# Kernel optimization log

Measured on AMD Instinct MI355X. Metric: run time of the kernel, lower is better.

Reference implementation:

```python
import jax, jax.numpy as jnp
import numpy as np

B, T, D, H = 4, 2048, 1024, 16
HD = D // H  # head_dim = 64

def setup_inputs() -> dict:
    key = jax.random.key(0)
    k1, k2, k3 = jax.random.split(key, 3)
    scale_in = 1.0 / np.sqrt(D)
    return {
        "x": jax.random.normal(k1, (B, T, D), dtype=jnp.float32),
        "W_qkv": jax.random.normal(k2, (D, 3 * D), dtype=jnp.float32) * scale_in,
        "b_qkv": jnp.zeros((3 * D,), dtype=jnp.float32),
        "W_out": jax.random.normal(k3, (D, D), dtype=jnp.float32) * scale_in,
        "b_out": jnp.zeros((D,), dtype=jnp.float32),
    }

def reference(x, W_qkv, b_qkv, W_out, b_out):
    Bx, Tx, C = x.shape
    qkv = x @ W_qkv + b_qkv                      # [B,T,3D]
    q, k, v = jnp.split(qkv, 3, axis=-1)
    # [B,T,D] -> [B,H,T,hd]
    def to_heads(t):
        return t.reshape(Bx, Tx, H, HD).transpose(0, 2, 1, 3)
    q, k, v = to_heads(q), to_heads(k), to_heads(v)
    scores = jnp.einsum('bhqd,bhkd->bhqk', q, k) / np.sqrt(HD)  # [B,H,T,T]
    causal = jnp.tril(jnp.ones((Tx, Tx), dtype=bool))
    scores = jnp.where(causal, scores, -jnp.inf)
    attn = jax.nn.softmax(scores, axis=-1)       # dropout p=0 -> identity
    out = jnp.einsum('bhqk,bhkd->bhqd', attn, v)  # [B,H,T,hd]
    out = out.transpose(0, 2, 1, 3).reshape(Bx, Tx, C)
    return out @ W_out + b_out
```

## Files before the change

kernel.cpp:

```cpp
#include <hip/hip_runtime.h>
#include <hip/hip_bf16.h>

#define BB 4
#define TT 2048
#define DD 1024
#define HH 16
#define HDIM 64
#define BT (BB*TT)
#define D3 (3*DD)

typedef __attribute__((ext_vector_type(8))) short bf16x8;
typedef __attribute__((ext_vector_type(4))) float f32x4;

#if __has_builtin(__builtin_amdgcn_exp2f)
#define EXP2(x) __builtin_amdgcn_exp2f(x)
#else
#define EXP2(x) exp2f(x)
#endif

__device__ __forceinline__ ushort f2bf(float f) {
  union { float f; uint32_t u; } v; v.f = f;
  uint32_t u = v.u + 0x7FFFu + ((v.u >> 16) & 1u);
  return (ushort)(u >> 16);
}

__device__ __forceinline__ ushort f2bf_hw(float f) {
  __hip_bfloat16 h = __float2bfloat16(f);
  ushort u;
  __builtin_memcpy(&u, &h, 2);
  return u;
}

__device__ __forceinline__ float bf2f(ushort u) {
  union { uint32_t i; float f; } x; x.i = ((uint32_t)u) << 16; return x.f;
}

__device__ __forceinline__ void gload_lds16(const void* g, void* l) {
  __builtin_amdgcn_global_load_lds((const __attribute__((address_space(1))) void*)g,
                                   (__attribute__((address_space(3))) void*)l, 16, 0, 0);
}

__global__ __launch_bounds__(256)
void cvt_bf16(const float* __restrict__ in, ushort* __restrict__ out, int n4) {
  int i = blockIdx.x * blockDim.x + threadIdx.x;
  int stride = gridDim.x * blockDim.x;
  for (; i < n4; i += stride) {
    float4 v = ((const float4*)in)[i];
    ushort4 o;
    o.x = f2bf(v.x); o.y = f2bf(v.y); o.z = f2bf(v.z); o.w = f2bf(v.w);
    ((ushort4*)out)[i] = o;
  }
}

__global__ __launch_bounds__(256)
void transpose_cvt(const float* __restrict__ W, ushort* __restrict__ Wt, int K, int N) {
  __shared__ ushort Tt[64][68];
  const int n0 = blockIdx.x * 64;
  const int k0 = blockIdx.y * 64;
  const int tid = threadIdx.x;
  const int r = tid >> 4;
  const int c4 = (tid & 15) * 4;
  #pragma unroll
  for (int i = 0; i < 4; ++i) {
    int row = r + i * 16;
    float4 v = *(const float4*)&W[(size_t)(k0 + row) * N + n0 + c4];
    Tt[c4 + 0][row] = f2bf(v.x);
    Tt[c4 + 1][row] = f2bf(v.y);
    Tt[c4 + 2][row] = f2bf(v.z);
    Tt[c4 + 3][row] = f2bf(v.w);
  }
  __syncthreads();
  #pragma unroll
  for (int i = 0; i < 4; ++i) {
    int row = r + i * 16;
    ushort4 tv = *(const ushort4*)&Tt[row][c4];
    *(ushort4*)&Wt[(size_t)(n0 + row) * K + k0 + c4] = tv;
  }
}

template<bool F32OUT>
__global__ __launch_bounds__(256)
void gemm_bt(const ushort* __restrict__ A, const ushort* __restrict__ Bw,
             const float* __restrict__ bias, void* __restrict__ C, int N) {
  __shared__ __align__(16) short As[128 * 64];
  __shared__ __align__(16) short Bs[128 * 64];
  const int tid = threadIdx.x;
  const int w = tid >> 6, lane = tid & 63;
  const int li = lane & 15, g = lane >> 4;
  const int wm = w >> 1, wn = w & 1;
  const int bm = blockIdx.y * 128;
  const int bn = blockIdx.x * 128;
  const int lrow = lane >> 3;
  const int lchunk = lane & 7;

  f32x4 acc[4][4] = {};

  for (int k0 = 0; k0 < 1024; k0 += 64) {
    __syncthreads();
    #pragma unroll
    for (int j = 0; j < 4; ++j) {
      int row = j * 32 + w * 8 + lrow;
      gload_lds16(A  + (size_t)(bm + row) * 1024 + k0 + lchunk * 8, As + j * 2048 + w * 512);
      gload_lds16(Bw + (size_t)(bn + row) * 1024 + k0 + lchunk * 8, Bs + j * 2048 + w * 512);
    }
    __syncthreads();
    #pragma unroll
    for (int c = 0; c < 2; ++c) {
      bf16x8 af[4], bfr[4];
      #pragma unroll
      for (int mi = 0; mi < 4; ++mi)
        af[mi] = *(bf16x8*)&As[(wm * 64 + mi * 16 + li) * 64 + c * 32 + g * 8];
      #pragma unroll
      for (int ni = 0; ni < 4; ++ni)
        bfr[ni] = *(bf16x8*)&Bs[(wn * 64 + ni * 16 + li) * 64 + c * 32 + g * 8];
      #pragma unroll
      for (int mi = 0; mi < 4; ++mi)
        #pragma unroll
        for (int ni = 0; ni < 4; ++ni)
          acc[mi][ni] = __builtin_amdgcn_mfma_f32_16x16x32_bf16(af[mi], bfr[ni], acc[mi][ni], 0, 0, 0);
    }
  }
  #pragma unroll
  for (int ni = 0; ni < 4; ++ni) {
    int col = bn + wn * 64 + ni * 16 + li;
    float bv = bias[col];
    #pragma unroll
    for (int mi = 0; mi < 4; ++mi) {
      int row = bm + wm * 64 + mi * 16 + g * 4;
      #pragma unroll
      for (int r = 0; r < 4; ++r) {
        float v = acc[mi][ni][r] + bv;
        if (F32OUT) ((float*)C)[(size_t)(row + r) * N + col] = v;
        else        ((ushort*)C)[(size_t)(row + r) * N + col] = f2bf_hw(v);
      }
    }
  }
}

__global__ void zero_ctr(uint* c) { *c = 0u; }

#define NITEMS 1024

__global__ __launch_bounds__(256)
void attn_mfma(const ushort* __restrict__ qkv, ushort* __restrict__ out,
               uint* __restrict__ ctr) {
  __shared__ __align__(16) short Ks[64 * 64];
  __shared__ __align__(16) short Vt[64 * 64];
  __shared__ __align__(16) short Pl[4 * 16 * 64];
  __shared__ int s_item;

  const int tid = threadIdx.x;
  const int w = tid >> 6;
  const int lane = tid & 63;
  const int li = lane & 15, g = lane >> 4;
  const int sw = (li & 7) << 4;

  char* KsB = (char*)Ks;
  char* VtB = (char*)Vt;
  char* PlB = (char*)Pl + w * 2048;

  const int krow0 = tid >> 3;
  const int kc = tid & 7;
  const int d0 = (tid >> 5) * 8;
  const int kp = tid & 31;
  const int kswz = (kc * 16) ^ ((krow0 & 7) << 4);

  for (;;) {
    if (tid == 0) s_item = (int)atomicAdd(ctr, 1u);
    __syncthreads();
    const int item = s_item;
    if (item >= NITEMS) return;

    const int qt = 15 - (item >> 6);
    const int bh = item & 63;
    const int h = bh & 15, b = bh >> 4;
    const int qg0 = qt * 128 + w * 32;

    bf16x8 qfr[2][2];
    #pragma unroll
    for (int qf = 0; qf < 2; ++qf) {
      const ushort* qrow = qkv + (size_t)(b * TT + qg0 + qf * 16 + li) * D3 + h * HDIM;
      #pragma unroll
      for (int c = 0; c < 2; ++c) {
        uint4 raw = *(const uint4*)(qrow + c * 32 + g * 8);
        const ushort* rp = (const ushort*)&raw;
        bf16x8 v;
        #pragma unroll
        for (int j = 0; j < 8; ++j)
          v[j] = (short)f2bf_hw(bf2f(rp[j]) * 0.18033688f);
        qfr[qf][c] = v;
      }
    }

    f32x4 o[4][2] = {};
    float lsum[2] = {0.f, 0.f};

    const ushort* kbase = qkv + (size_t)b * TT * D3 + DD + h * HDIM;
    const ushort* vbase = kbase + DD;

    const int nt = 2 * qt + 2;
    const int itlast = 2 * qt + (w >> 1);

    uint4 kpre0, kpre1, vpre0, vpre1;
    {
      const ushort* kg = kbase + (size_t)krow0 * D3 + kc * 8;
      kpre0 = *(const uint4*)kg;
      kpre1 = *(const uint4*)(kg + (size_t)32 * D3);
      const ushort* vg = vbase + (size_t)(2 * kp) * D3 + d0;
      vpre0 = *(const uint4*)vg;
      vpre1 = *(const uint4*)(vg + D3);
    }

    for (int it = 0; it < nt; ++it) {
      const int k0 = it * 64;
      *(uint4*)(KsB + krow0 * 128 + kswz) = kpre0;
      *(uint4*)(KsB + (krow0 + 32) * 128 + kswz) = kpre1;
      {
        const ushort* pa = (const ushort*)&vpre0;
        const ushort* pb = (const ushort*)&vpre1;
        #pragma unroll
        for (int j = 0; j < 8; ++j) {
          uint32_t pk = (uint32_t)pa[j] | ((uint32_t)pb[j] << 16);
          *(uint32_t*)(VtB + (d0 + j) * 128 + ((4 * kp) ^ (j << 4))) = pk;
        }
      }
      __syncthreads();
      if (it + 1 < nt) {
        const ushort* kg = kbase + (size_t)(k0 + 64 + krow0) * D3 + kc * 8;
        kpre0 = *(const uint4*)kg;
        kpre1 = *(const uint4*)(kg + (size_t)32 * D3);
        const ushort* vg = vbase + (size_t)(k0 + 64 + 2 * kp) * D3 + d0;
        vpre0 = *(const uint4*)vg;
        vpre1 = *(const uint4*)(vg + D3);
      }
      if (it <= itlast) {
        const bool domask = (it == itlast);
        bf16x8 pf[2][2];
        f32x4 s[2][4];
        __builtin_amdgcn_s_setprio(1);
        #pragma unroll
        for (int kt = 0; kt < 4; ++kt) {
          const int row = kt * 16 + li;
          bf16x8 kf0 = *(bf16x8*)(KsB + row * 128 + ((g * 16) ^ sw));
          bf16x8 kf1 = *(bf16x8*)(KsB + row * 128 + ((64 + g * 16) ^ sw));
          #pragma unroll
          for (int qf = 0; qf < 2; ++qf) {
            f32x4 a = {0.f, 0.f, 0.f, 0.f};
            a = __builtin_amdgcn_mfma_f32_16x16x32_bf16(kf0, qfr[qf][0], a, 0, 0, 0);
            a = __builtin_amdgcn_mfma_f32_16x16x32_bf16(kf1, qfr[qf][1], a, 0, 0, 0);
            s[qf][kt] = a;
          }
        }
        __builtin_amdgcn_s_setprio(0);
        #pragma unroll
        for (int qf = 0; qf < 2; ++qf) {
          const int qrow = qg0 + qf * 16 + li;
          if (domask) {
            #pragma unroll
            for (int kt = 0; kt < 4; ++kt)
              #pragma unroll
              for (int r = 0; r < 4; ++r) {
                int key = k0 + kt * 16 + g * 4 + r;
                if (key > qrow) s[qf][kt][r] = -1e30f;
              }
          }
          float ls = 0.f;
          #pragma unroll
          for (int kt = 0; kt < 4; ++kt) {
            float p0 = EXP2(s[qf][kt][0]);
            float p1 = EXP2(s[qf][kt][1]);
            float p2 = EXP2(s[qf][kt][2]);
            float p3 = EXP2(s[qf][kt][3]);
            ls += (p0 + p1) + (p2 + p3);
            uint2 val;
            val.x = (uint32_t)f2bf_hw(p0) | ((uint32_t)f2bf_hw(p1) << 16);
            val.y = (uint32_t)f2bf_hw(p2) | ((uint32_t)f2bf_hw(p3) << 16);
            *(uint2*)(PlB + li * 128 + ((kt * 32 + g * 8) ^ sw)) = val;
          }
          lsum[qf] += ls;
          pf[qf][0] = *(bf16x8*)(PlB + li * 128 + ((g * 16) ^ sw));
          pf[qf][1] = *(bf16x8*)(PlB + li * 128 + ((64 + g * 16) ^ sw));
        }
        __builtin_amdgcn_s_setprio(1);
        #pragma unroll
        for (int dt = 0; dt < 4; ++dt) {
          const int vrow = dt * 16 + li;
          bf16x8 vf0 = *(bf16x8*)(VtB + vrow * 128 + ((g * 16) ^ sw));
          bf16x8 vf1 = *(bf16x8*)(VtB + vrow * 128 + ((64 + g * 16) ^ sw));
          #pragma unroll
          for (int qf = 0; qf < 2; ++qf) {
            o[dt][qf] = __builtin_amdgcn_mfma_f32_16x16x32_bf16(vf0, pf[qf][0], o[dt][qf], 0, 0, 0);
            o[dt][qf] = __builtin_amdgcn_mfma_f32_16x16x32_bf16(vf1, pf[qf][1], o[dt][qf], 0, 0, 0);
          }
        }
        __builtin_amdgcn_s_setprio(0);
      }
      __syncthreads();
    }

    #pragma unroll
    for (int qf = 0; qf < 2; ++qf) {
      float lt = lsum[qf];
      lt += __shfl_xor(lt, 16);
      lt += __shfl_xor(lt, 32);
      float inv = 1.f / lt;
      ushort* orow = out + (size_t)(b * TT + qg0 + qf * 16 + li) * DD + h * HDIM;
      #pragma unroll
      for (int dt = 0; dt < 4; ++dt) {
        uint2 pk;
        pk.x = (uint32_t)f2bf_hw(o[dt][qf][0] * inv) | ((uint32_t)f2bf_hw(o[dt][qf][1] * inv) << 16);
        pk.y = (uint32_t)f2bf_hw(o[dt][qf][2] * inv) | ((uint32_t)f2bf_hw(o[dt][qf][3] * inv) << 16);
        *(uint2*)&orow[dt * 16 + g * 4] = pk;
      }
    }
  }
}

extern "C" void kernel_launch(void* const* d_in, const int* in_sizes, int n_in,
                              void* d_out, int out_size, void* d_ws, size_t ws_size,
                              hipStream_t stream) {
  const float* x     = (const float*)d_in[0];
  const float* W_qkv = (const float*)d_in[1];
  const float* b_qkv = (const float*)d_in[2];
  const float* W_out = (const float*)d_in[3];
  const float* b_out = (const float*)d_in[4];
  float* out = (float*)d_out;

  ushort* x_bf   = (ushort*)d_ws;
  ushort* wtq    = x_bf + (size_t)BT * DD;
  ushort* wto    = wtq + (size_t)D3 * DD;
  ushort* qkv_bf = wto + (size_t)DD * DD;
  ushort* att_bf = qkv_bf + (size_t)BT * D3;
  uint*   ctr    = (uint*)(att_bf + (size_t)BT * DD);

  zero_ctr<<<1, 1, 0, stream>>>(ctr);
  cvt_bf16<<<2048, 256, 0, stream>>>(x, x_bf, BT * DD / 4);
  transpose_cvt<<<dim3(D3 / 64, DD / 64), 256, 0, stream>>>(W_qkv, wtq, DD, D3);
  transpose_cvt<<<dim3(DD / 64, DD / 64), 256, 0, stream>>>(W_out, wto, DD, DD);

  gemm_bt<false><<<dim3(D3 / 128, BT / 128), 256, 0, stream>>>(x_bf, wtq, b_qkv, (void*)qkv_bf, D3);
  attn_mfma<<<dim3(1024), 256, 0, stream>>>(qkv_bf, att_bf, ctr);
  gemm_bt<true><<<dim3(DD / 128, BT / 128), 256, 0, stream>>>(att_bf, wto, b_out, (void*)out, DD);
}
```

Before: 201.1 us.

## Use 256x256-tile 8-wave double-buffered GEMM for QKV projection

Replaces the QKV projection GEMM with a new kernel that uses 512 threads (8 waves), 256x256 output tiles and a double-buffered LDS pipeline fed by direct global-to-LDS loads. The next K-slice is prefetched while MFMAs run, and compute is split into phases separated by barriers, with s_setprio raising wave priority during MFMA bursts. The aim is more operand reuse per LDS byte and better overlap of memory with compute. It uses 128KB of LDS per block and only 384 blocks, which limits occupancy and can leave CUs unevenly loaded.

New measurement: 192.0 us. 1.05x faster.

```diff
diff --git a/kernel.cpp b/kernel.cpp
--- a/kernel.cpp
+++ b/kernel.cpp
@@ -133,6 +133,126 @@
         if (F32OUT) ((float*)C)[(size_t)(row + r) * N + col] = v;
         else        ((ushort*)C)[(size_t)(row + r) * N + col] = f2bf_hw(v);
       }
+    }
+  }
+}
+
+__global__ __launch_bounds__(512, 2)
+void gemm_qkv_8p(const ushort* __restrict__ A, const ushort* __restrict__ Bw,
+                 const float* __restrict__ bias, ushort* __restrict__ C, int N) {
+  __shared__ __align__(16) short lds[4 * 256 * 64];
+
+  const int tid = threadIdx.x;
+  const int w = tid >> 6;
+  const int wm = w >> 2;
+  const int wn = w & 3;
+  const int lane = tid & 63;
+  const int li = lane & 15, g = lane >> 4;
+  const int swz = (li & 7) << 4;
+
+  const int bm = blockIdx.y * 256;
+  const int bn = blockIdx.x * 256;
+  const ushort* Ag = A + (size_t)bm * 1024;
+  const ushort* Bg = Bw + (size_t)bn * 1024;
+
+  const int lrow8 = lane >> 3;
+  const int chsw = (lane & 7) ^ lrow8;
+
+  f32x4 acc[8][4] = {};
+
+#define STAGE8(t, p) do { \
+  const int kk_ = (t) * 64; \
+  short* Ad_ = lds + (p) * 32768; \
+  short* Bd_ = Ad_ + 16384; \
+  _Pragma("unroll") \
+  for (int h_ = 0; h_ < 2; ++h_) { \
+    _Pragma("unroll") \
+    for (int j_ = 0; j_ < 2; ++j_) { \
+      const int r_ = h_ * 128 + w * 16 + j_ * 8; \
+      gload_lds16(Ag + (size_t)(r_ + lrow8) * 1024 + kk_ + chsw * 8, Ad_ + r_ * 64); \
+      gload_lds16(Bg + (size_t)(r_ + lrow8) * 1024 + kk_ + chsw * 8, Bd_ + r_ * 64); \
+    } \
+  } \
+} while (0)
+
+  STAGE8(0, 0);
+  asm volatile("s_waitcnt vmcnt(0)" ::: "memory");
+  __builtin_amdgcn_sched_barrier(0);
+  __builtin_amdgcn_s_barrier();
+
+  for (int s = 0; s < 16; ++s) {
+    const int cur = s & 1;
+    const char* Ab = (const char*)lds + cur * 65536;
+    const char* Bb = Ab + 32768;
+
+    if (s + 1 < 16) STAGE8(s + 1, cur ^ 1);
+
+    bf16x8 af[8], bf[4];
+    #pragma unroll
+    for (int mi = 0; mi < 8; ++mi)
+      af[mi] = *(const bf16x8*)(Ab + (wm * 128 + mi * 16 + li) * 128 + ((g * 16) ^ swz));
+    #pragma unroll
+    for (int ni = 0; ni < 2; ++ni)
+      bf[ni] = *(const bf16x8*)(Bb + (wn * 64 + ni * 16 + li) * 128 + ((g * 16) ^ swz));
+    __builtin_amdgcn_s_setprio(1);
+    #pragma unroll
+    for (int mi = 0; mi < 8; ++mi)
+      #pragma unroll
+      for (int ni = 0; ni < 2; ++ni)
+        acc[mi][ni] = __builtin_amdgcn_mfma_f32_16x16x32_bf16(af[mi], bf[ni], acc[mi][ni], 0, 0, 0);
+    __builtin_amdgcn_s_setprio(0);
+    __builtin_amdgcn_s_barrier();
+    #pragma unroll
+    for (int ni = 2; ni < 4; ++ni)
+      bf[ni] = *(const bf16x8*)(Bb + (wn * 64 + ni * 16 + li) * 128 + ((g * 16) ^ swz));
+    __builtin_amdgcn_s_setprio(1);
+    #pragma unroll
+    for (int mi = 0; mi < 8; ++mi)
+      #pragma unroll
+      for (int ni = 2; ni < 4; ++ni)
+        acc[mi][ni] = __builtin_amdgcn_mfma_f32_16x16x32_bf16(af[mi], bf[ni], acc[mi][ni], 0, 0, 0);
+    __builtin_amdgcn_s_setprio(0);
+    __builtin_amdgcn_s_barrier();
+    #pragma unroll
+    for (int mi = 0; mi < 8; ++mi)
+      af[mi] = *(const bf16x8*)(Ab + (wm * 128 + mi * 16 + li) * 128 + ((64 + g * 16) ^ swz));
+    #pragma unroll
+    for (int ni = 0; ni < 2; ++ni)
+      bf[ni] = *(const bf16x8*)(Bb + (wn * 64 + ni * 16 + li) * 128 + ((64 + g * 16) ^ swz));
+    __builtin_amdgcn_s_setprio(1);
+    #pragma unroll
+    for (int mi = 0; mi < 8; ++mi)
+      #pragma unroll
+      for (int ni = 0; ni < 2; ++ni)
+        acc[mi][ni] = __builtin_amdgcn_mfma_f32_16x16x32_bf16(af[mi], bf[ni], acc[mi][ni], 0, 0, 0);
+    __builtin_amdgcn_s_setprio(0);
+    __builtin_amdgcn_s_barrier();
+    #pragma unroll
+    for (int ni = 2; ni < 4; ++ni)
+      bf[ni] = *(const bf16x8*)(Bb + (wn * 64 + ni * 16 + li) * 128 + ((64 + g * 16) ^ swz));
+    __builtin_amdgcn_s_setprio(1);
+    #pragma unroll
+    for (int mi = 0; mi < 8; ++mi)
+      #pragma unroll
+      for (int ni = 2; ni < 4; ++ni)
+        acc[mi][ni] = __builtin_amdgcn_mfma_f32_16x16x32_bf16(af[mi], bf[ni], acc[mi][ni], 0, 0, 0);
+    __builtin_amdgcn_s_setprio(0);
+    asm volatile("s_waitcnt vmcnt(0)" ::: "memory");
+    __builtin_amdgcn_sched_barrier(0);
+    __builtin_amdgcn_s_barrier();
+  }
+#undef STAGE8
+
+  #pragma unroll
+  for (int ni = 0; ni < 4; ++ni) {
+    int col = bn + wn * 64 + ni * 16 + li;
+    float bv = bias[col];
+    #pragma unroll
+    for (int mi = 0; mi < 8; ++mi) {
+      int row = bm + wm * 128 + mi * 16 + g * 4;
+      #pragma unroll
+      for (int r = 0; r < 4; ++r)
+        C[(size_t)(row + r) * N + col] = f2bf_hw(acc[mi][ni][r] + bv);
     }
   }
 }
@@ -338,7 +458,7 @@
   transpose_cvt<<<dim3(D3 / 64, DD / 64), 256, 0, stream>>>(W_qkv, wtq, DD, D3);
   transpose_cvt<<<dim3(DD / 64, DD / 64), 256, 0, stream>>>(W_out, wto, DD, DD);
 
-  gemm_bt<false><<<dim3(D3 / 128, BT / 128), 256, 0, stream>>>(x_bf, wtq, b_qkv, (void*)qkv_bf, D3);
+  gemm_qkv_8p<<<dim3(D3 / 256, BT / 256), 512, 0, stream>>>(x_bf, wtq, b_qkv, qkv_bf, D3);
   attn_mfma<<<dim3(1024), 256, 0, stream>>>(qkv_bf, att_bf, ctr);
   gemm_bt<true><<<dim3(DD / 128, BT / 128), 256, 0, stream>>>(att_bf, wto, b_out, (void*)out, DD);
 }
```

## Add double-buffered 8-wave QKV GEMM with swizzled LDS and fold counter reset

Applied to the files above, without the earlier changes.

Replaces the QKV projection GEMM with a new 512-thread kernel using 128x256 tiles. It double-buffers K-slices in LDS so the next tile's global-to-LDS loads overlap the current tile's MFMA work, applies an XOR swizzle to reduce LDS bank conflicts, and raises wave priority around the MFMA bursts. The counter-zeroing launch is folded into the conversion kernel, which removes one kernel launch, and the existing GEMM gains an explicit vmcnt wait before its barrier. The costs are higher LDS use (96KB per block) and more register pressure, which may limit occupancy.

Result: faster. 185.4 us (-7.8%).

```diff
diff --git a/kernel.cpp b/kernel.cpp
--- a/kernel.cpp
+++ b/kernel.cpp
@@ -41,7 +41,9 @@
 }
 
 __global__ __launch_bounds__(256)
-void cvt_bf16(const float* __restrict__ in, ushort* __restrict__ out, int n4) {
+void cvt_bf16(const float* __restrict__ in, ushort* __restrict__ out, int n4,
+              uint* __restrict__ ctr) {
+  if (blockIdx.x == 0 && threadIdx.x == 0) *ctr = 0u;
   int i = blockIdx.x * blockDim.x + threadIdx.x;
   int stride = gridDim.x * blockDim.x;
   for (; i < n4; i += stride) {
@@ -103,6 +105,8 @@
       gload_lds16(A  + (size_t)(bm + row) * 1024 + k0 + lchunk * 8, As + j * 2048 + w * 512);
       gload_lds16(Bw + (size_t)(bn + row) * 1024 + k0 + lchunk * 8, Bs + j * 2048 + w * 512);
     }
+    asm volatile("s_waitcnt vmcnt(0)" ::: "memory");
+    __builtin_amdgcn_sched_barrier(0);
     __syncthreads();
     #pragma unroll
     for (int c = 0; c < 2; ++c) {
@@ -137,7 +141,94 @@
   }
 }
 
-__global__ void zero_ctr(uint* c) { *c = 0u; }
+__global__ __launch_bounds__(512, 2)
+void gemm_qkv_8p(const ushort* __restrict__ A, const ushort* __restrict__ Bw,
+                 const float* __restrict__ bias, ushort* __restrict__ C, int N) {
+  __shared__ __align__(16) short lds[2 * (128 + 256) * 64];
+
+  const int tid = threadIdx.x;
+  const int w = tid >> 6;
+  const int wm = w >> 2;
+  const int wn = w & 3;
+  const int lane = tid & 63;
+  const int li = lane & 15, g = lane >> 4;
+  const int swz = (li & 7) << 4;
+
+  const int bm = blockIdx.y * 128;
+  const int bn = blockIdx.x * 256;
+  const ushort* Ag = A + (size_t)bm * 1024;
+  const ushort* Bg = Bw + (size_t)bn * 1024;
+
+  const int lrow8 = lane >> 3;
+  const int chsw = (lane & 7) ^ lrow8;
+
+  f32x4 acc[4][4] = {};
+
+#define STAGE6(t, p) do { \
+  const int kk_ = (t) * 64; \
+  short* Ad_ = lds + (p) * 24576; \
+  short* Bd_ = Ad_ + 8192; \
+  _Pragma("unroll") \
+  for (int h_ = 0; h_ < 2; ++h_) { \
+    const int r_ = h_ * 64 + w * 8; \
+    gload_lds16(Ag + (size_t)(r_ + lrow8) * 1024 + kk_ + chsw * 8, Ad_ + r_ * 64); \
+  } \
+  _Pragma("unroll") \
+  for (int j_ = 0; j_ < 4; ++j_) { \
+    const int r_ = j_ * 64 + w * 8; \
+    gload_lds16(Bg + (size_t)(r_ + lrow8) * 1024 + kk_ + chsw * 8, Bd_ + r_ * 64); \
+  } \
+} while (0)
+
+  STAGE6(0, 0);
+  asm volatile("s_waitcnt vmcnt(0)" ::: "memory");
+  __builtin_amdgcn_sched_barrier(0);
+  __builtin_amdgcn_s_barrier();
+
+  for (int s = 0; s < 16; ++s) {
+    const int cur = s & 1;
+    const char* Ab = (const char*)lds + cur * 49152;
+    const char* Bb = Ab + 16384;
+
+    if (s + 1 < 16) STAGE6(s + 1, cur ^ 1);
+
+    #pragma unroll
+    for (int kh = 0; kh < 2; ++kh) {
+      bf16x8 af[4], bf[4];
+      #pragma unroll
+      for (int mi = 0; mi < 4; ++mi)
+        af[mi] = *(const bf16x8*)(Ab + (wm * 64 + mi * 16 + li) * 128 + ((kh * 64 + g * 16) ^ swz));
+      #pragma unroll
+      for (int ni = 0; ni < 4; ++ni)
+        bf[ni] = *(const bf16x8*)(Bb + (wn * 64 + ni * 16 + li) * 128 + ((kh * 64 + g * 16) ^ swz));
+      __builtin_amdgcn_s_setprio(1);
+      #pragma unroll
+      for (int mi = 0; mi < 4; ++mi)
+        #pragma unroll
+        for (int ni = 0; ni < 4; ++ni)
+          acc[mi][ni] = __builtin_amdgcn_mfma_f32_16x16x32_bf16(af[mi], bf[ni], acc[mi][ni], 0, 0, 0);
+      __builtin_amdgcn_s_setprio(0);
+      if (kh == 0) __builtin_amdgcn_s_barrier();
+    }
+    asm volatile("s_waitcnt vmcnt(0)" ::: "memory");
+    __builtin_amdgcn_sched_barrier(0);
+    __builtin_amdgcn_s_barrier();
+  }
+#undef STAGE6
+
+  #pragma unroll
+  for (int ni = 0; ni < 4; ++ni) {
+    int col = bn + wn * 64 + ni * 16 + li;
+    float bv = bias[col];
+    #pragma unroll
+    for (int mi = 0; mi < 4; ++mi) {
+      int row = bm + wm * 64 + mi * 16 + g * 4;
+      #pragma unroll
+      for (int r = 0; r < 4; ++r)
+        C[(size_t)(row + r) * N + col] = f2bf_hw(acc[mi][ni][r] + bv);
+    }
+  }
+}
 
 #define NITEMS 1024
 
@@ -333,12 +424,11 @@
   ushort* att_bf = qkv_bf + (size_t)BT * D3;
   uint*   ctr    = (uint*)(att_bf + (size_t)BT * DD);
 
-  zero_ctr<<<1, 1, 0, stream>>>(ctr);
-  cvt_bf16<<<2048, 256, 0, stream>>>(x, x_bf, BT * DD / 4);
+  cvt_bf16<<<2048, 256, 0, stream>>>(x, x_bf, BT * DD / 4, ctr);
   transpose_cvt<<<dim3(D3 / 64, DD / 64), 256, 0, stream>>>(W_qkv, wtq, DD, D3);
   transpose_cvt<<<dim3(DD / 64, DD / 64), 256, 0, stream>>>(W_out, wto, DD, DD);
 
-  gemm_bt<false><<<dim3(D3 / 128, BT / 128), 256, 0, stream>>>(x_bf, wtq, b_qkv, (void*)qkv_bf, D3);
+  gemm_qkv_8p<<<dim3(D3 / 256, BT / 128), 512, 0, stream>>>(x_bf, wtq, b_qkv, qkv_bf, D3);
   attn_mfma<<<dim3(1024), 256, 0, stream>>>(qkv_bf, att_bf, ctr);
   gemm_bt<true><<<dim3(DD / 128, BT / 128), 256, 0, stream>>>(att_bf, wto, b_out, (void*)out, DD);
 }
```
